# Kernel optimization log

Measured on AMD Instinct MI355X. Metric: run time of the kernel, lower is better.

## Reference

```python
import jax, jax.numpy as jnp
import numpy as np

EMBED_DIM = 1024
NUM_HEADS = 16
HEAD_DIM = EMBED_DIM // NUM_HEADS
EPSILON = 1e-6
SCORE_SCALE = 1.0
B, L = 2, 2048


def setup_inputs() -> dict:
    key = jax.random.key(0)
    k0, k1, k2, k3, k4 = jax.random.split(key, 5)
    s_in = 1.0 / np.sqrt(EMBED_DIM)
    return {
        "x": jax.random.normal(k0, (B, L, EMBED_DIM), dtype=jnp.float32),
        "w_qkv": jax.random.normal(k1, (EMBED_DIM, 3 * EMBED_DIM), dtype=jnp.float32) * s_in,
        "b_qkv": jnp.zeros((3 * EMBED_DIM,), dtype=jnp.float32),
        "w_out": jax.random.normal(k2, (EMBED_DIM, EMBED_DIM), dtype=jnp.float32) * s_in,
        "b_out": jnp.zeros((EMBED_DIM,), dtype=jnp.float32),
    }


def reference(x, w_qkv, b_qkv, w_out, b_out):
    Bq, Lq, E = x.shape
    qkv = x @ w_qkv + b_qkv  # [B, L, 3E]
    q, k, v = jnp.split(qkv, 3, axis=-1)
    q = q.reshape(Bq, Lq, NUM_HEADS, HEAD_DIM).transpose(0, 2, 1, 3)  # bhld
    k = k.reshape(Bq, Lq, NUM_HEADS, HEAD_DIM).transpose(0, 2, 1, 3)
    v = v.reshape(Bq, Lq, NUM_HEADS, HEAD_DIM).transpose(0, 2, 1, 3)

    dot = jnp.einsum('bhid,bhjd->bhij', q, k)
    q_norm_sq = jnp.sum(q * q, axis=-1, keepdims=True)          # [b,h,L,1]
    k_norm_sq = jnp.sum(k * k, axis=-1, keepdims=True)          # [b,h,L,1]
    vals = q_norm_sq + k_norm_sq.transpose(0, 1, 3, 2)          # [b,h,L,L]
    scores = (dot * dot) / (vals - 2.0 * dot + EPSILON) * SCORE_SCALE

    mask = jnp.triu(jnp.ones((Lq, Lq), dtype=scores.dtype), k=1) * -1e9
    scores = scores + mask[None, None, :, :]
    attn = jax.nn.softmax(scores, axis=-1)
    out = jnp.einsum('bhij,bhjd->bhid', attn, v)
    out = out.transpose(0, 2, 1, 3).reshape(Bq, Lq, E)
    return out @ w_out + b_out
```

## Files before the change

### kernel.cpp

```cpp
#include <hip/hip_runtime.h>

#define EMBED 1024
#define NH 16
#define HD 64
#define SEQ 2048
#define BATCH 2
#define ROWS (BATCH*SEQ)
#define BHD (BATCH*NH)

typedef __bf16 bf16x8 __attribute__((ext_vector_type(8)));
typedef _Float16 f16x4 __attribute__((ext_vector_type(4)));
typedef float f32x4 __attribute__((ext_vector_type(4)));

__device__ __forceinline__ unsigned short f2bf(float f){
  union { float f; unsigned u; } v; v.f = f;
  unsigned r = v.u + 0x7fffu + ((v.u >> 16) & 1u);
  return (unsigned short)(r >> 16);
}
__device__ __forceinline__ float bf2f(unsigned short s){
  union { unsigned u; float f; } v; v.u = ((unsigned)s) << 16; return v.f;
}
__device__ __forceinline__ unsigned short f2h(float f){
  union { _Float16 h; unsigned short u; } v; v.h = (_Float16)f; return v.u;
}

typedef __attribute__((address_space(1))) unsigned int as1_t;
typedef __attribute__((address_space(3))) unsigned int as3_t;
__device__ __forceinline__ void async_ld16(const void* gp, void* lp){
  __builtin_amdgcn_global_load_lds((as1_t*)gp, (as3_t*)lp, 16, 0, 0);
}


__global__ __launch_bounds__(256) void k_conv(const float* __restrict__ x,
                                              unsigned short* __restrict__ xb, int n4){
  int i = blockIdx.x * blockDim.x + threadIdx.x;
  if (i < n4){
    float4 f = ((const float4*)x)[i];
    ushort4 o;
    o.x = f2bf(f.x); o.y = f2bf(f.y); o.z = f2bf(f.z); o.w = f2bf(f.w);
    ((ushort4*)xb)[i] = o;
  }
}

__global__ __launch_bounds__(256) void k_tr_f2b(const float* __restrict__ in,
                                                unsigned short* __restrict__ out, int R, int C){
  __shared__ float t[32][33];
  int c0 = blockIdx.x * 32, r0 = blockIdx.y * 32;
  int tx = threadIdx.x, ty = threadIdx.y;
  #pragma unroll
  for (int i = 0; i < 4; i++){ int r = ty + i*8; t[r][tx] = in[(size_t)(r0+r)*C + c0 + tx]; }
  __syncthreads();
  #pragma unroll
  for (int i = 0; i < 4; i++){ int rr = ty + i*8; out[(size_t)(c0+rr)*R + r0 + tx] = f2bf(t[tx][rr]); }
}

__global__ __launch_bounds__(256) void k_tr_b2b(const unsigned short* __restrict__ in,
                                                unsigned short* __restrict__ out, int R, int C){
  in  += (size_t)blockIdx.z * R * C;
  out += (size_t)blockIdx.z * R * C;
  __shared__ unsigned short t[32][33];
  int c0 = blockIdx.x * 32, r0 = blockIdx.y * 32;
  int tx = threadIdx.x, ty = threadIdx.y;
  #pragma unroll
  for (int i = 0; i < 4; i++){ int r = ty + i*8; t[r][tx] = in[(size_t)(r0+r)*C + c0 + tx]; }
  __syncthreads();
  #pragma unroll
  for (int i = 0; i < 4; i++){ int rr = ty + i*8; out[(size_t)(c0+rr)*R + r0 + tx] = t[tx][rr]; }
}

__global__ __launch_bounds__(256) void k_norms(const unsigned short* __restrict__ q,
                                               const unsigned short* __restrict__ k,
                                               float* __restrict__ qn, float* __restrict__ kn){
  int i = blockIdx.x * blockDim.x + threadIdx.x;
  const uint4* qr = (const uint4*)(q + (size_t)i * HD);
  const uint4* kr = (const uint4*)(k + (size_t)i * HD);
  float sq = 0.f, sk = 0.f;
  #pragma unroll
  for (int t = 0; t < 8; t++){
    uint4 uq = qr[t], uk = kr[t];
    unsigned aq[4] = {uq.x, uq.y, uq.z, uq.w};
    unsigned ak[4] = {uk.x, uk.y, uk.z, uk.w};
    #pragma unroll
    for (int j = 0; j < 4; j++){
      float f0 = bf2f((unsigned short)(aq[j] & 0xffff));
      float f1 = bf2f((unsigned short)(aq[j] >> 16));
      sq += f0*f0 + f1*f1;
      float g0 = bf2f((unsigned short)(ak[j] & 0xffff));
      float g1 = bf2f((unsigned short)(ak[j] >> 16));
      sk += g0*g0 + g1*g1;
    }
  }
  qn[i] = sq; kn[i] = sk;
}


__global__ __launch_bounds__(256) void k_gemm_qkv(
    const unsigned short* __restrict__ A,
    const unsigned short* __restrict__ BT,
    const float* __restrict__ bias,
    unsigned short* __restrict__ qo, unsigned short* __restrict__ ko,
    unsigned short* __restrict__ vo)
{
  __shared__ __align__(16) unsigned short As[128*32];
  __shared__ __align__(16) unsigned short Bs[128*32];
  const int K = EMBED;
  int m0 = blockIdx.x * 128, n0 = blockIdx.y * 128;
  int tid = threadIdx.x, lane = tid & 63, wave = tid >> 6;
  int wm = wave >> 1, wn = wave & 1;
  int l16 = lane & 15, quad = lane >> 4;
  f32x4 acc[4][4] = {};
  int c0i = wave*64 + lane, c1i = 256 + wave*64 + lane;
  int r0 = c0i >> 2, cc0 = (c0i & 3) * 8;
  int r1 = c1i >> 2, cc1 = (c1i & 3) * 8;
  unsigned short* lA0 = &As[(wave*64)*8];
  unsigned short* lA1 = &As[(256 + wave*64)*8];
  unsigned short* lB0 = &Bs[(wave*64)*8];
  unsigned short* lB1 = &Bs[(256 + wave*64)*8];
  for (int k0 = 0; k0 < K; k0 += 32){
    async_ld16((void*)&A [(size_t)(m0 + r0)*K + k0 + cc0], (void*)lA0);
    async_ld16((void*)&A [(size_t)(m0 + r1)*K + k0 + cc1], (void*)lA1);
    async_ld16((void*)&BT[(size_t)(n0 + r0)*K + k0 + cc0], (void*)lB0);
    async_ld16((void*)&BT[(size_t)(n0 + r1)*K + k0 + cc1], (void*)lB1);
    __syncthreads();
    bf16x8 af[4], bfr[4];
    #pragma unroll
    for (int mi = 0; mi < 4; mi++) af[mi]  = *(const bf16x8*)&As[(wm*64 + mi*16 + l16)*32 + quad*8];
    #pragma unroll
    for (int ni = 0; ni < 4; ni++) bfr[ni] = *(const bf16x8*)&Bs[(wn*64 + ni*16 + l16)*32 + quad*8];
    #pragma unroll
    for (int mi = 0; mi < 4; mi++)
      #pragma unroll
      for (int ni = 0; ni < 4; ni++)
        acc[mi][ni] = __builtin_amdgcn_mfma_f32_16x16x32_bf16(af[mi], bfr[ni], acc[mi][ni], 0, 0, 0);
    __syncthreads();
  }
  #pragma unroll
  for (int mi = 0; mi < 4; mi++)
    #pragma unroll
    for (int ni = 0; ni < 4; ni++)
      #pragma unroll
      for (int rr = 0; rr < 4; rr++){
        int row = m0 + wm*64 + mi*16 + quad*4 + rr;
        int col = n0 + wn*64 + ni*16 + l16;
        float val = acc[mi][ni][rr] + bias[col];
        int b = row >> 11, l = row & 2047;
        int which = col >> 10, e = col & 1023, h = e >> 6, d = e & 63;
        unsigned short* dst = which == 0 ? qo : (which == 1 ? ko : vo);
        unsigned short bits = (which == 2) ? f2h(val) : f2bf(val);
        dst[(((size_t)(b*NH + h))*SEQ + l)*HD + d] = bits;
      }
}


__global__ __launch_bounds__(128) void k_attn(
    const unsigned short* __restrict__ qg,
    const unsigned short* __restrict__ kg,
    const unsigned short* __restrict__ vtg,
    const float* __restrict__ qn,
    const float* __restrict__ kn,
    unsigned short* __restrict__ attn_out)
{
  __shared__ __align__(16) unsigned short Ks[2][32*72];
  __shared__ __align__(16) _Float16      Vs[2][64*36];
  int bh = blockIdx.y; int b = bh >> 4, h = bh & 15;
  int tid = threadIdx.x, lane = tid & 63, wave = tid >> 6;
  int l16 = lane & 15, quad = lane >> 4;
  int p = blockIdx.x;

  const unsigned short* qbase = qg  + (size_t)bh * SEQ * HD;
  const unsigned short* kbase = kg  + (size_t)bh * SEQ * HD;
  const _Float16*       vtb   = (const _Float16*)vtg + (size_t)bh * HD * SEQ;
  const float* knb = kn + (size_t)bh * SEQ;

  int kd0 = tid >> 3,        kc0 = tid & 7;
  int kd1 = (tid + 128) >> 3, kc1 = tid & 7;
  int vd0 = tid >> 2,        vc0 = tid & 3;
  int vd1 = 32 + (tid >> 2), vc1 = tid & 3;

  #pragma unroll
  for (int pass = 0; pass < 2; pass++){
    int t = pass ? (63 - p) : p;
    int q0 = t*32 + wave*16;
    int jmax_w = q0 + 16;
    int jmax_b = t*32 + 32;

    bf16x8 aq[2];
    #pragma unroll
    for (int sk = 0; sk < 2; sk++)
      aq[sk] = *(const bf16x8*)&qbase[(size_t)(q0 + l16)*HD + sk*32 + quad*8];
    float qn_m = qn[(size_t)bh*SEQ + q0 + l16];

    float m_run = -1e30f, l_lane = 0.f;
    f32x4 oacc[4] = {};

    {
      uint4 ka = *(const uint4*)&kbase[(size_t)kd0*HD + kc0*8];
      uint4 kb = *(const uint4*)&kbase[(size_t)kd1*HD + kc1*8];
      uint4 va = *(const uint4*)&vtb[(size_t)vd0*SEQ + vc0*8];
      uint4 vb = *(const uint4*)&vtb[(size_t)vd1*SEQ + vc1*8];
      *(uint4*)&Ks[0][kd0*72 + kc0*8] = ka;
      *(uint4*)&Ks[0][kd1*72 + kc1*8] = kb;
      *(uint2*)&Vs[0][vd0*36 + vc0*8]     = make_uint2(va.x, va.y);
      *(uint2*)&Vs[0][vd0*36 + vc0*8 + 4] = make_uint2(va.z, va.w);
      *(uint2*)&Vs[0][vd1*36 + vc1*8]     = make_uint2(vb.x, vb.y);
      *(uint2*)&Vs[0][vd1*36 + vc1*8 + 4] = make_uint2(vb.z, vb.w);
    }
    __syncthreads();

    for (int j0 = 0; j0 < jmax_b; j0 += 32){
      int buf = (j0 >> 5) & 1;
      int jn = (j0 + 32 < jmax_b) ? j0 + 32 : j0;
      uint4 ka = *(const uint4*)&kbase[(size_t)(jn + kd0)*HD + kc0*8];
      uint4 kb = *(const uint4*)&kbase[(size_t)(jn + kd1)*HD + kc1*8];
      uint4 va = *(const uint4*)&vtb[(size_t)vd0*SEQ + jn + vc0*8];
      uint4 vb = *(const uint4*)&vtb[(size_t)vd1*SEQ + jn + vc1*8];

      if (j0 < jmax_w){
        f32x4 st[2] = {};
        #pragma unroll
        for (int tile = 0; tile < 2; tile++)
          #pragma unroll
          for (int sk = 0; sk < 2; sk++){
            bf16x8 ak = *(const bf16x8*)&Ks[buf][(tile*16 + l16)*72 + (sk*4 + quad)*8];
            st[tile] = __builtin_amdgcn_mfma_f32_16x16x32_bf16(ak, aq[sk], st[tile], 0, 0, 0);
          }
        float4 kn_a = *(const float4*)&knb[j0 + quad*4];
        float4 kn_b = *(const float4*)&knb[j0 + 16 + quad*4];
        float kn_j[2][4] = {{kn_a.x, kn_a.y, kn_a.z, kn_a.w}, {kn_b.x, kn_b.y, kn_b.z, kn_b.w}};
        int mg = q0 + l16;
        float sc[2][4];
        if (j0 + 32 > q0){
          #pragma unroll
          for (int tile = 0; tile < 2; tile++)
            #pragma unroll
            for (int rr = 0; rr < 4; rr++){
              int jg = j0 + tile*16 + quad*4 + rr;
              float dot = st[tile][rr];
              float den = fmaxf(qn_m + kn_j[tile][rr] - 2.0f*dot, 0.0f) + 1e-6f;
              float v = dot * dot * __builtin_amdgcn_rcpf(den);
              sc[tile][rr] = (jg <= mg) ? v : -1e30f;
            }
        } else {
          #pragma unroll
          for (int tile = 0; tile < 2; tile++)
            #pragma unroll
            for (int rr = 0; rr < 4; rr++){
              float dot = st[tile][rr];
              float den = fmaxf(qn_m + kn_j[tile][rr] - 2.0f*dot, 0.0f) + 1e-6f;
              sc[tile][rr] = dot * dot * __builtin_amdgcn_rcpf(den);
            }
        }
        float mx = fmaxf(fmaxf(fmaxf(sc[0][0], sc[0][1]), fmaxf(sc[0][2], sc[0][3])),
                         fmaxf(fmaxf(sc[1][0], sc[1][1]), fmaxf(sc[1][2], sc[1][3])));
        mx = fmaxf(mx, __shfl_xor(mx, 16));
        mx = fmaxf(mx, __shfl_xor(mx, 32));
        float mnew = fmaxf(m_run, mx);
        float alpha = __expf(m_run - mnew);
        m_run = mnew;

        float ps = 0.f;
        #pragma unroll
        for (int tile = 0; tile < 2; tile++)
          #pragma unroll
          for (int rr = 0; rr < 4; rr++){
            float e = __expf(sc[tile][rr] - mnew);
            sc[tile][rr] = e; ps += e;
          }
        l_lane = l_lane * alpha + ps;

        #pragma unroll
        for (int g = 0; g < 4; g++)
          #pragma unroll
          for (int rr = 0; rr < 4; rr++) oacc[g][rr] *= alpha;

        #pragma unroll
        for (int tile = 0; tile < 2; tile++){
          f16x4 pf;
          #pragma unroll
          for (int rr = 0; rr < 4; rr++) pf[rr] = (_Float16)sc[tile][rr];
          #pragma unroll
          for (int g = 0; g < 4; g++){
            f16x4 av = *(const f16x4*)&Vs[buf][(g*16 + l16)*36 + (tile*4 + quad)*4];
            oacc[g] = __builtin_amdgcn_mfma_f32_16x16x16f16(av, pf, oacc[g], 0, 0, 0);
          }
        }
      }

      *(uint4*)&Ks[buf^1][kd0*72 + kc0*8] = ka;
      *(uint4*)&Ks[buf^1][kd1*72 + kc1*8] = kb;
      *(uint2*)&Vs[buf^1][vd0*36 + vc0*8]     = make_uint2(va.x, va.y);
      *(uint2*)&Vs[buf^1][vd0*36 + vc0*8 + 4] = make_uint2(va.z, va.w);
      *(uint2*)&Vs[buf^1][vd1*36 + vc1*8]     = make_uint2(vb.x, vb.y);
      *(uint2*)&Vs[buf^1][vd1*36 + vc1*8 + 4] = make_uint2(vb.z, vb.w);
      __syncthreads();
    }

    float l_tot = l_lane + __shfl_xor(l_lane, 16);
    l_tot += __shfl_xor(l_tot, 32);
    float linv = __builtin_amdgcn_rcpf(l_tot);

    size_t orow = (size_t)(b*SEQ + q0 + l16)*EMBED + h*HD;
    #pragma unroll
    for (int g = 0; g < 4; g++){
      ushort4 pk;
      pk.x = f2bf(oacc[g][0] * linv);
      pk.y = f2bf(oacc[g][1] * linv);
      pk.z = f2bf(oacc[g][2] * linv);
      pk.w = f2bf(oacc[g][3] * linv);
      *(ushort4*)&attn_out[orow + g*16 + quad*4] = pk;
    }
    __syncthreads();
  }
}


__global__ __launch_bounds__(256) void k_gemm_out(
    const unsigned short* __restrict__ A,
    const unsigned short* __restrict__ BT,
    const float* __restrict__ bias,
    float* __restrict__ out)
{
  __shared__ __align__(16) unsigned short As[128*32];
  __shared__ __align__(16) unsigned short Bs[128*32];
  const int K = EMBED;
  int m0 = blockIdx.x * 128, n0 = blockIdx.y * 128;
  int tid = threadIdx.x, lane = tid & 63, wave = tid >> 6;
  int wm = wave >> 1, wn = wave & 1;
  int l16 = lane & 15, quad = lane >> 4;
  f32x4 acc[4][4] = {};
  int c0i = wave*64 + lane, c1i = 256 + wave*64 + lane;
  int r0 = c0i >> 2, cc0 = (c0i & 3) * 8;
  int r1 = c1i >> 2, cc1 = (c1i & 3) * 8;
  unsigned short* lA0 = &As[(wave*64)*8];
  unsigned short* lA1 = &As[(256 + wave*64)*8];
  unsigned short* lB0 = &Bs[(wave*64)*8];
  unsigned short* lB1 = &Bs[(256 + wave*64)*8];
  for (int k0 = 0; k0 < K; k0 += 32){
    async_ld16((void*)&A [(size_t)(m0 + r0)*K + k0 + cc0], (void*)lA0);
    async_ld16((void*)&A [(size_t)(m0 + r1)*K + k0 + cc1], (void*)lA1);
    async_ld16((void*)&BT[(size_t)(n0 + r0)*K + k0 + cc0], (void*)lB0);
    async_ld16((void*)&BT[(size_t)(n0 + r1)*K + k0 + cc1], (void*)lB1);
    __syncthreads();
    bf16x8 af[4], bfr[4];
    #pragma unroll
    for (int mi = 0; mi < 4; mi++) af[mi]  = *(const bf16x8*)&As[(wm*64 + mi*16 + l16)*32 + quad*8];
    #pragma unroll
    for (int ni = 0; ni < 4; ni++) bfr[ni] = *(const bf16x8*)&Bs[(wn*64 + ni*16 + l16)*32 + quad*8];
    #pragma unroll
    for (int mi = 0; mi < 4; mi++)
      #pragma unroll
      for (int ni = 0; ni < 4; ni++)
        acc[mi][ni] = __builtin_amdgcn_mfma_f32_16x16x32_bf16(af[mi], bfr[ni], acc[mi][ni], 0, 0, 0);
    __syncthreads();
  }
  #pragma unroll
  for (int mi = 0; mi < 4; mi++)
    #pragma unroll
    for (int ni = 0; ni < 4; ni++)
      #pragma unroll
      for (int rr = 0; rr < 4; rr++){
        int row = m0 + wm*64 + mi*16 + quad*4 + rr;
        int col = n0 + wn*64 + ni*16 + l16;
        out[(size_t)row*EMBED + col] = acc[mi][ni][rr] + bias[col];
      }
}


extern "C" void kernel_launch(void* const* d_in, const int* in_sizes, int n_in,
                              void* d_out, int out_size, void* d_ws, size_t ws_size,
                              hipStream_t stream) {
  const float* x     = (const float*)d_in[0];
  const float* w_qkv = (const float*)d_in[1];
  const float* b_qkv = (const float*)d_in[2];
  const float* w_out = (const float*)d_in[3];
  const float* b_out = (const float*)d_in[4];
  float* out = (float*)d_out;

  char* ws = (char*)d_ws;
  size_t off = 0;
  auto alloc = [&](size_t bytes) -> void* {
    void* p = ws + off; off += (bytes + 255) & ~(size_t)255; return p;
  };
  unsigned short* xb    = (unsigned short*)alloc((size_t)ROWS * EMBED * 2);
  unsigned short* wqkvT = (unsigned short*)alloc((size_t)3 * EMBED * EMBED * 2);
  unsigned short* woutT = (unsigned short*)alloc((size_t)EMBED * EMBED * 2);
  unsigned short* qb    = (unsigned short*)alloc((size_t)ROWS * EMBED * 2);
  unsigned short* kb    = (unsigned short*)alloc((size_t)ROWS * EMBED * 2);
  unsigned short* vb    = (unsigned short*)alloc((size_t)ROWS * EMBED * 2);
  unsigned short* vTb   = (unsigned short*)alloc((size_t)ROWS * EMBED * 2);
  float* qn = (float*)alloc((size_t)BHD * SEQ * 4);
  float* kn = (float*)alloc((size_t)BHD * SEQ * 4);
  unsigned short* attnb = xb;

  k_conv<<<dim3((ROWS*EMBED/4 + 255)/256), dim3(256), 0, stream>>>(x, xb, ROWS*EMBED/4);
  k_tr_f2b<<<dim3(3*EMBED/32, EMBED/32), dim3(32, 8), 0, stream>>>(w_qkv, wqkvT, EMBED, 3*EMBED);
  k_tr_f2b<<<dim3(EMBED/32, EMBED/32), dim3(32, 8), 0, stream>>>(w_out, woutT, EMBED, EMBED);
  k_gemm_qkv<<<dim3(ROWS/128, 3*EMBED/128), dim3(256), 0, stream>>>(xb, wqkvT, b_qkv, qb, kb, vb);
  k_norms<<<dim3(BHD*SEQ/256), dim3(256), 0, stream>>>(qb, kb, qn, kn);
  k_tr_b2b<<<dim3(HD/32, SEQ/32, BHD), dim3(32, 8), 0, stream>>>(vb, vTb, SEQ, HD);
  k_attn<<<dim3(32, BHD), dim3(128), 0, stream>>>(qb, kb, vTb, qn, kn, attnb);
  k_gemm_out<<<dim3(ROWS/128, EMBED/128), dim3(256), 0, stream>>>(attnb, woutT, b_out, out);
}
```

Measured before the change: 246.6 us.

## Split attention key range into two halves with partial outputs and combine kernel

Each attention query tile's causal key range is split into two halves handled by separate blocks, doubling the grid from 1024 to 2048 blocks. Each block writes unnormalized fp32 partial outputs plus running max and sum, and a new combine kernel merges them with softmax rescaling into the bf16 attention output. This aims to raise occupancy and parallelism on the many-CU GPU, at the cost of extra global traffic for partials and an additional kernel launch. Launch bounds also request 4 blocks per CU.

```diff
diff --git a/kernel.cpp b/kernel.cpp
--- a/kernel.cpp
+++ b/kernel.cpp
@@ -152,37 +152,41 @@
 }
 
 
-__global__ __launch_bounds__(128) void k_attn(
+__global__ __launch_bounds__(128, 4) void k_attn(
     const unsigned short* __restrict__ qg,
     const unsigned short* __restrict__ kg,
     const unsigned short* __restrict__ vtg,
     const float* __restrict__ qn,
     const float* __restrict__ kn,
-    unsigned short* __restrict__ attn_out)
+    float* __restrict__ Opart,
+    float* __restrict__ Mp,
+    float* __restrict__ Lp)
 {
   __shared__ __align__(16) unsigned short Ks[2][32*72];
   __shared__ __align__(16) _Float16      Vs[2][64*36];
-  int bh = blockIdx.y; int b = bh >> 4, h = bh & 15;
+  int bh = blockIdx.y;
   int tid = threadIdx.x, lane = tid & 63, wave = tid >> 6;
   int l16 = lane & 15, quad = lane >> 4;
-  int p = blockIdx.x;
+  int P = blockIdx.x >> 1, s = blockIdx.x & 1;
 
   const unsigned short* qbase = qg  + (size_t)bh * SEQ * HD;
   const unsigned short* kbase = kg  + (size_t)bh * SEQ * HD;
   const _Float16*       vtb   = (const _Float16*)vtg + (size_t)bh * HD * SEQ;
   const float* knb = kn + (size_t)bh * SEQ;
 
-  int kd0 = tid >> 3,        kc0 = tid & 7;
+  int kd0 = tid >> 3,         kc0 = tid & 7;
   int kd1 = (tid + 128) >> 3, kc1 = tid & 7;
-  int vd0 = tid >> 2,        vc0 = tid & 3;
-  int vd1 = 32 + (tid >> 2), vc1 = tid & 3;
+  int vd0 = tid >> 2,         vc0 = tid & 3;
+  int vd1 = 32 + (tid >> 2),  vc1 = tid & 3;
 
   #pragma unroll
   for (int pass = 0; pass < 2; pass++){
-    int t = pass ? (63 - p) : p;
+    int t = pass ? (63 - P) : P;
+    int nj = t + 1;
+    int half = (nj + 1) >> 1;
+    int jb_lo = s ? half : 0;
+    int jb_hi = s ? nj : half;
     int q0 = t*32 + wave*16;
-    int jmax_w = q0 + 16;
-    int jmax_b = t*32 + 32;
 
     bf16x8 aq[2];
     #pragma unroll
@@ -193,29 +197,31 @@
     float m_run = -1e30f, l_lane = 0.f;
     f32x4 oacc[4] = {};
 
-    {
-      uint4 ka = *(const uint4*)&kbase[(size_t)kd0*HD + kc0*8];
-      uint4 kb = *(const uint4*)&kbase[(size_t)kd1*HD + kc1*8];
-      uint4 va = *(const uint4*)&vtb[(size_t)vd0*SEQ + vc0*8];
-      uint4 vb = *(const uint4*)&vtb[(size_t)vd1*SEQ + vc1*8];
-      *(uint4*)&Ks[0][kd0*72 + kc0*8] = ka;
-      *(uint4*)&Ks[0][kd1*72 + kc1*8] = kb;
-      *(uint2*)&Vs[0][vd0*36 + vc0*8]     = make_uint2(va.x, va.y);
-      *(uint2*)&Vs[0][vd0*36 + vc0*8 + 4] = make_uint2(va.z, va.w);
-      *(uint2*)&Vs[0][vd1*36 + vc1*8]     = make_uint2(vb.x, vb.y);
-      *(uint2*)&Vs[0][vd1*36 + vc1*8 + 4] = make_uint2(vb.z, vb.w);
-    }
-    __syncthreads();
-
-    for (int j0 = 0; j0 < jmax_b; j0 += 32){
-      int buf = (j0 >> 5) & 1;
-      int jn = (j0 + 32 < jmax_b) ? j0 + 32 : j0;
-      uint4 ka = *(const uint4*)&kbase[(size_t)(jn + kd0)*HD + kc0*8];
-      uint4 kb = *(const uint4*)&kbase[(size_t)(jn + kd1)*HD + kc1*8];
-      uint4 va = *(const uint4*)&vtb[(size_t)vd0*SEQ + jn + vc0*8];
-      uint4 vb = *(const uint4*)&vtb[(size_t)vd1*SEQ + jn + vc1*8];
-
-      if (j0 < jmax_w){
+    if (jb_lo < jb_hi){
+      int jlo = jb_lo * 32;
+      {
+        uint4 ka = *(const uint4*)&kbase[(size_t)(jlo + kd0)*HD + kc0*8];
+        uint4 kb = *(const uint4*)&kbase[(size_t)(jlo + kd1)*HD + kc1*8];
+        uint4 va = *(const uint4*)&vtb[(size_t)vd0*SEQ + jlo + vc0*8];
+        uint4 vb = *(const uint4*)&vtb[(size_t)vd1*SEQ + jlo + vc1*8];
+        *(uint4*)&Ks[0][kd0*72 + kc0*8] = ka;
+        *(uint4*)&Ks[0][kd1*72 + kc1*8] = kb;
+        *(uint2*)&Vs[0][vd0*36 + vc0*8]     = make_uint2(va.x, va.y);
+        *(uint2*)&Vs[0][vd0*36 + vc0*8 + 4] = make_uint2(va.z, va.w);
+        *(uint2*)&Vs[0][vd1*36 + vc1*8]     = make_uint2(vb.x, vb.y);
+        *(uint2*)&Vs[0][vd1*36 + vc1*8 + 4] = make_uint2(vb.z, vb.w);
+      }
+      __syncthreads();
+
+      for (int jb = jb_lo; jb < jb_hi; jb++){
+        int j0 = jb * 32;
+        int buf = (jb - jb_lo) & 1;
+        int jn = (jb + 1 < jb_hi) ? (jb + 1)*32 : j0;
+        uint4 ka = *(const uint4*)&kbase[(size_t)(jn + kd0)*HD + kc0*8];
+        uint4 kb = *(const uint4*)&kbase[(size_t)(jn + kd1)*HD + kc1*8];
+        uint4 va = *(const uint4*)&vtb[(size_t)vd0*SEQ + jn + vc0*8];
+        uint4 vb = *(const uint4*)&vtb[(size_t)vd1*SEQ + jn + vc1*8];
+
         f32x4 st[2] = {};
         #pragma unroll
         for (int tile = 0; tile < 2; tile++)
@@ -284,32 +290,60 @@
             oacc[g] = __builtin_amdgcn_mfma_f32_16x16x16f16(av, pf, oacc[g], 0, 0, 0);
           }
         }
+
+        *(uint4*)&Ks[buf^1][kd0*72 + kc0*8] = ka;
+        *(uint4*)&Ks[buf^1][kd1*72 + kc1*8] = kb;
+        *(uint2*)&Vs[buf^1][vd0*36 + vc0*8]     = make_uint2(va.x, va.y);
+        *(uint2*)&Vs[buf^1][vd0*36 + vc0*8 + 4] = make_uint2(va.z, va.w);
+        *(uint2*)&Vs[buf^1][vd1*36 + vc1*8]     = make_uint2(vb.x, vb.y);
+        *(uint2*)&Vs[buf^1][vd1*36 + vc1*8 + 4] = make_uint2(vb.z, vb.w);
+        __syncthreads();
       }
-
-      *(uint4*)&Ks[buf^1][kd0*72 + kc0*8] = ka;
-      *(uint4*)&Ks[buf^1][kd1*72 + kc1*8] = kb;
-      *(uint2*)&Vs[buf^1][vd0*36 + vc0*8]     = make_uint2(va.x, va.y);
-      *(uint2*)&Vs[buf^1][vd0*36 + vc0*8 + 4] = make_uint2(va.z, va.w);
-      *(uint2*)&Vs[buf^1][vd1*36 + vc1*8]     = make_uint2(vb.x, vb.y);
-      *(uint2*)&Vs[buf^1][vd1*36 + vc1*8 + 4] = make_uint2(vb.z, vb.w);
-      __syncthreads();
     }
 
     float l_tot = l_lane + __shfl_xor(l_lane, 16);
     l_tot += __shfl_xor(l_tot, 32);
-    float linv = __builtin_amdgcn_rcpf(l_tot);
-
-    size_t orow = (size_t)(b*SEQ + q0 + l16)*EMBED + h*HD;
+
+    int r = wave*16 + l16;
+    size_t pb = ((size_t)(bh*64 + t)*2 + s) * (32*64);
     #pragma unroll
     for (int g = 0; g < 4; g++){
-      ushort4 pk;
-      pk.x = f2bf(oacc[g][0] * linv);
-      pk.y = f2bf(oacc[g][1] * linv);
-      pk.z = f2bf(oacc[g][2] * linv);
-      pk.w = f2bf(oacc[g][3] * linv);
-      *(ushort4*)&attn_out[orow + g*16 + quad*4] = pk;
+      float4 pk = make_float4(oacc[g][0], oacc[g][1], oacc[g][2], oacc[g][3]);
+      *(float4*)&Opart[pb + (size_t)r*64 + g*16 + quad*4] = pk;
+    }
+    if (quad == 0){
+      int mb = ((bh*64 + t)*2 + s)*32 + r;
+      Mp[mb] = m_run;
+      Lp[mb] = l_tot;
     }
     __syncthreads();
+  }
+}
+
+
+__global__ __launch_bounds__(256) void k_combine(
+    const float* __restrict__ Opart,
+    const float* __restrict__ Mp,
+    const float* __restrict__ Lp,
+    unsigned short* __restrict__ attn_out)
+{
+  int t = blockIdx.x;
+  int bh = blockIdx.y; int b = bh >> 4, h = bh & 15;
+  int tid = threadIdx.x;
+  int d = tid & 63, r8 = (tid >> 6) * 8;
+  size_t i0 = ((size_t)(bh*64 + t)*2) * 2048;
+  size_t i1 = i0 + 2048;
+  int mb = ((bh*64 + t)*2) * 32;
+  #pragma unroll
+  for (int rr = 0; rr < 8; rr++){
+    int r = r8 + rr;
+    float m0 = Mp[mb + r],      m1 = Mp[mb + 32 + r];
+    float l0 = Lp[mb + r],      l1 = Lp[mb + 32 + r];
+    float ms = fmaxf(m0, m1);
+    float w0 = __expf(m0 - ms), w1 = __expf(m1 - ms);
+    float den = w0*l0 + w1*l1;
+    float o = (w0*Opart[i0 + (size_t)r*64 + d] + w1*Opart[i1 + (size_t)r*64 + d]) / den;
+    attn_out[(size_t)(b*SEQ + t*32 + r)*EMBED + h*HD + d] = f2bf(o);
   }
 }
 
@@ -390,6 +424,9 @@
   unsigned short* vTb   = (unsigned short*)alloc((size_t)ROWS * EMBED * 2);
   float* qn = (float*)alloc((size_t)BHD * SEQ * 4);
   float* kn = (float*)alloc((size_t)BHD * SEQ * 4);
+  float* Opart = (float*)alloc((size_t)BHD * 64 * 2 * 32 * 64 * 4);
+  float* Mp    = (float*)alloc((size_t)BHD * 64 * 2 * 32 * 4);
+  float* Lp    = (float*)alloc((size_t)BHD * 64 * 2 * 32 * 4);
   unsigned short* attnb = xb;
 
   k_conv<<<dim3((ROWS*EMBED/4 + 255)/256), dim3(256), 0, stream>>>(x, xb, ROWS*EMBED/4);
@@ -398,6 +435,7 @@
   k_gemm_qkv<<<dim3(ROWS/128, 3*EMBED/128), dim3(256), 0, stream>>>(xb, wqkvT, b_qkv, qb, kb, vb);
   k_norms<<<dim3(BHD*SEQ/256), dim3(256), 0, stream>>>(qb, kb, qn, kn);
   k_tr_b2b<<<dim3(HD/32, SEQ/32, BHD), dim3(32, 8), 0, stream>>>(vb, vTb, SEQ, HD);
-  k_attn<<<dim3(32, BHD), dim3(128), 0, stream>>>(qb, kb, vTb, qn, kn, attnb);
+  k_attn<<<dim3(64, BHD), dim3(128), 0, stream>>>(qb, kb, vTb, qn, kn, Opart, Mp, Lp);
+  k_combine<<<dim3(64, BHD), dim3(256), 0, stream>>>(Opart, Mp, Lp, attnb);
   k_gemm_out<<<dim3(ROWS/128, EMBED/128), dim3(256), 0, stream>>>(attnb, woutT, b_out, out);
 }
```

Result: faster. 222.4 us (-9.8%).
